# Optimization experiments

Measured on AMD Instinct MI355X. Metric: run time of the kernel, lower is better.

Reference implementation:

```python
import jax, jax.numpy as jnp
import numpy as np

EPS = 1e-6
ROPE_BASE = 10000.0


def rms_norm(x, gamma):
    # normalize over last dim (head_dim)
    var = jnp.mean(x * x, axis=-1, keepdims=True)
    return x * jax.lax.rsqrt(var + EPS) * gamma


def apply_rope(x):
    # x: [B, L, nH, hd]; rotate-half RoPE over flattened sequence positions
    L, hd = x.shape[1], x.shape[-1]
    half = hd // 2
    inv_freq = 1.0 / (ROPE_BASE ** (jnp.arange(half, dtype=jnp.float32) / half))
    ang = jnp.arange(L, dtype=jnp.float32)[:, None] * inv_freq[None, :]  # [L, half]
    cos = jnp.cos(ang)[None, :, None, :]
    sin = jnp.sin(ang)[None, :, None, :]
    x1, x2 = x[..., :half], x[..., half:]
    return jnp.concatenate([x1 * cos - x2 * sin, x1 * sin + x2 * cos], axis=-1)


def setup_inputs() -> dict:
    key = jax.random.key(0)
    k1, k2, k3 = jax.random.split(key, 3)
    B, H, W, C = 8, 32, 32, 768
    x = jax.random.normal(k1, (B, H, W, C), dtype=jnp.float32)
    w_qkv = jax.random.normal(k2, (3 * C, C), dtype=jnp.float32) * (1.0 / np.sqrt(C))
    w_out = jax.random.normal(k3, (C, C), dtype=jnp.float32) * (1.0 / np.sqrt(C))
    q_gamma = jnp.ones((64,), dtype=jnp.float32)
    k_gamma = jnp.ones((64,), dtype=jnp.float32)
    return {"x": x, "w_qkv": w_qkv, "q_gamma": q_gamma, "k_gamma": k_gamma, "w_out": w_out}


def reference(x, w_qkv, q_gamma, k_gamma, w_out):
    B, H, W, C = x.shape
    nH = 12
    hd = C // nH
    L = H * W
    x_flat = x.reshape(B, L, C)
    qkv = jnp.einsum('blc,dc->bld', x_flat, w_qkv).reshape(B, L, 3, nH, hd)
    q, k, v = qkv[:, :, 0], qkv[:, :, 1], qkv[:, :, 2]  # [B, L, nH, hd]
    q = apply_rope(rms_norm(q, q_gamma))
    k = apply_rope(rms_norm(k, k_gamma))
    scale = 1.0 / np.sqrt(hd)
    scores = jnp.einsum('bqhd,bkhd->bhqk', q, k) * scale
    attn = jax.nn.softmax(scores, axis=-1)
    out = jnp.einsum('bhqk,bkhd->bqhd', attn, v).reshape(B, H, W, C)
    return jnp.einsum('bhwc,dc->bhwd', out, w_out)
```

## Files before the change

kernel.cpp:

```cpp
#include <hip/hip_runtime.h>
#include <math.h>

#define NB 8
#define SL 1024
#define CD 768
#define NHH 12
#define HD 64
#define QKVD 2304

typedef __attribute__((ext_vector_type(8))) __bf16 bf16x8;
typedef __attribute__((ext_vector_type(8))) unsigned short u16x8;
typedef __attribute__((ext_vector_type(4))) float f32x4;
typedef __attribute__((ext_vector_type(16))) float f32x16;
typedef __attribute__((ext_vector_type(4))) unsigned int u32x4;
#define MFMA16(a, b, c) __builtin_amdgcn_mfma_f32_16x16x32_bf16(a, b, c, 0, 0, 0)
#define MFMA32(a, b, c) __builtin_amdgcn_mfma_f32_32x32x16_bf16(a, b, c, 0, 0, 0)

__host__ __device__ __forceinline__ float bf2f(unsigned short u) {
  union { unsigned int i; float f; } v; v.i = ((unsigned int)u) << 16; return v.f;
}
__host__ __device__ __forceinline__ unsigned short f2bf(float f) {
  union { float ff; unsigned int i; } v; v.ff = f;
  unsigned int x = v.i;
  x += 0x7FFFu + ((x >> 16) & 1u);
  return (unsigned short)(x >> 16);
}
__device__ __forceinline__ unsigned int pkbf(float a, float b) {
  unsigned short ua = __builtin_bit_cast(unsigned short, (__bf16)a);
  unsigned short ub = __builtin_bit_cast(unsigned short, (__bf16)b);
  return ((unsigned int)ub << 16) | ua;
}

__device__ __forceinline__ void gload_lds16(const void* g, void* l) {
  __builtin_amdgcn_global_load_lds(
      (const __attribute__((address_space(1))) unsigned int*)g,
      (__attribute__((address_space(3))) unsigned int*)l, 16, 0, 0);
}

__global__ __launch_bounds__(256) void conv_kernel(
    const float4* __restrict__ in, ushort4* __restrict__ out, int n4)
{
  int i = blockIdx.x * 256 + threadIdx.x;
  if (i < n4) {
    float4 v = in[i];
    ushort4 o;
    o.x = f2bf(v.x); o.y = f2bf(v.y); o.z = f2bf(v.z); o.w = f2bf(v.w);
    out[i] = o;
  }
}

template <int CF32>
__global__ __launch_bounds__(256) void gemm_mfma(
    const unsigned short* __restrict__ A, const unsigned short* __restrict__ B,
    void* __restrict__ Cv, int M, int N, int K)
{
  __shared__ alignas(16) unsigned short AsL[128 * 32];
  __shared__ alignas(16) unsigned short BsL[128 * 32];
  const int m0 = blockIdx.y * 128, n0 = blockIdx.x * 128;
  const int t = threadIdx.x;
  const int wave = t >> 6, lane = t & 63;
  const int wm = (wave >> 1) * 64, wn = (wave & 1) * 64;
  const int lm = lane & 15, quad = lane >> 4;
  f32x4 acc[4][4];
#pragma unroll
  for (int i = 0; i < 4; ++i)
#pragma unroll
    for (int j = 0; j < 4; ++j)
#pragma unroll
      for (int r = 0; r < 4; ++r) acc[i][j][r] = 0.f;

  const int sr = t >> 2, sc = (t & 3) * 8;
  const unsigned short* ag = A + (size_t)(m0 + sr) * K + sc;
  const unsigned short* bg = B + (size_t)(n0 + sr) * K + sc;
  for (int k0 = 0; k0 < K; k0 += 32) {
    gload_lds16(ag + k0, &AsL[t * 8]);
    gload_lds16(ag + (size_t)64 * K + k0, &AsL[2048 + t * 8]);
    gload_lds16(bg + k0, &BsL[t * 8]);
    gload_lds16(bg + (size_t)64 * K + k0, &BsL[2048 + t * 8]);
    __syncthreads();
    bf16x8 af[4], bfr[4];
#pragma unroll
    for (int i = 0; i < 4; ++i)
      af[i] = *(const bf16x8*)&AsL[(wm + i * 16 + lm) * 32 + quad * 8];
#pragma unroll
    for (int j = 0; j < 4; ++j)
      bfr[j] = *(const bf16x8*)&BsL[(wn + j * 16 + lm) * 32 + quad * 8];
#pragma unroll
    for (int i = 0; i < 4; ++i)
#pragma unroll
      for (int j = 0; j < 4; ++j)
        acc[i][j] = MFMA16(af[i], bfr[j], acc[i][j]);
    __syncthreads();
  }
#pragma unroll
  for (int i = 0; i < 4; ++i) {
    const int row = m0 + wm + i * 16 + quad * 4;
#pragma unroll
    for (int r = 0; r < 4; ++r) {
      const size_t base = (size_t)(row + r) * N + n0 + wn + lm;
#pragma unroll
      for (int j = 0; j < 4; ++j) {
        if (CF32) ((float*)Cv)[base + j * 16] = acc[i][j][r];
        else ((unsigned short*)Cv)[base + j * 16] = f2bf(acc[i][j][r]);
      }
    }
  }
}

__global__ __launch_bounds__(256) void rmsrope_kernel(
    unsigned short* __restrict__ qkv,
    const float* __restrict__ qg, const float* __restrict__ kg)
{
  const int wid  = (int)((blockIdx.x * blockDim.x + threadIdx.x) >> 6);
  const int lane = threadIdx.x & 63;
  const int h = wid % NHH;
  const int s = (wid / NHH) & 1;
  const int l = (wid / (2 * NHH)) % SL;
  const int b = wid / (2 * NHH * SL);
  unsigned short* p = qkv + (((size_t)(b * SL + l) * 3 + s) * NHH + h) * HD + lane;
  float v = bf2f(*p);
  float ss = v * v;
#pragma unroll
  for (int off = 32; off; off >>= 1) ss += __shfl_xor(ss, off);
  float g = s ? kg[lane] : qg[lane];
  v = v * rsqrtf(ss * (1.0f / 64.0f) + 1e-6f) * g;
  float partner = __shfl_xor(v, 32);
  const int j = lane & 31;
  float ang = (float)l * exp2f((float)j * (-13.287712379549449f / 32.0f));
  float sn, cs;
  sincosf(ang, &sn, &cs);
  *p = f2bf((lane < 32) ? (v * cs - partner * sn) : (partner * sn + v * cs));
}

__global__ __launch_bounds__(256) void attn_mfma(
    const unsigned short* __restrict__ qkv, unsigned short* __restrict__ ctx)
{
  __shared__ alignas(16) unsigned short KsL[2][64 * 64];
  __shared__ alignas(16) unsigned short Vt[2][64][76];
  const int bid = (int)(blockIdx.x + 8 * (blockIdx.y + 12 * blockIdx.z));
  const int nb = (bid & 7) * 96 + (bid >> 3);
  const int qt = nb & 7;
  const int h = (nb >> 3) % 12;
  const int b = nb / 96;
  const int t = threadIdx.x, wave = t >> 6, lane = t & 63;
  const int q_l = lane & 31, hi = lane >> 5;
  const int wq = wave * 32;
  const int vkey = t & 63, vds = (t >> 6) * 16;
  const int kr = t >> 3, kc = t & 7;
  const float SCALE = 0.125f * 1.44269504088896340736f;

  const unsigned short* base_k = qkv + (size_t)b * SL * QKVD + (NHH * HD) + h * HD;
  const unsigned short* base_v = qkv + (size_t)b * SL * QKVD + 2 * (NHH * HD) + h * HD;

  bf16x8 qf[4];
  {
    const unsigned short* qp =
        qkv + (((size_t)(b * SL + qt * 128 + wq + q_l) * 3 + 0) * NHH + h) * HD + hi * 8;
#pragma unroll
    for (int ds = 0; ds < 4; ++ds) qf[ds] = *(const bf16x8*)(qp + ds * 16);
  }
  f32x16 o0, o1;
#pragma unroll
  for (int r = 0; r < 16; ++r) { o0[r] = 0.f; o1[r] = 0.f; }
  float m_i = -INFINITY, l_i = 0.f;

  const int ksw = (kc ^ (kr & 7)) * 8;
#define STAGE_K(KT, BUF)                                                      \
  {                                                                           \
    const unsigned short* k0p = base_k + (size_t)((KT)*64 + kr) * QKVD + ksw; \
    gload_lds16(k0p, &KsL[BUF][t * 8]);                                       \
    const unsigned short* k1p =                                               \
        base_k + (size_t)((KT)*64 + 32 + kr) * QKVD + ksw;                    \
    gload_lds16(k1p, &KsL[BUF][2048 + t * 8]);                                \
  }

  STAGE_K(0, 0);
  {
    const unsigned short* vp = base_v + (size_t)vkey * QKVD + vds;
    u16x8 v0 = *(const u16x8*)(vp);
    u16x8 v1 = *(const u16x8*)(vp + 8);
#pragma unroll
    for (int e = 0; e < 8; ++e) {
      Vt[0][vds + e][vkey] = v0[e];
      Vt[0][vds + 8 + e][vkey] = v1[e];
    }
  }
  __syncthreads();

  for (int kt = 0; kt < 16; ++kt) {
    const int cur = kt & 1, nxt = cur ^ 1;
    const int ktn = (kt + 1) & 15;
    STAGE_K(ktn, nxt);
    const unsigned short* vp = base_v + (size_t)(ktn * 64 + vkey) * QKVD + vds;
    u16x8 v0n = *(const u16x8*)(vp);
    u16x8 v1n = *(const u16x8*)(vp + 8);
    const unsigned short* Kb = KsL[cur];
    f32x16 st0, st1;
#pragma unroll
    for (int r = 0; r < 16; ++r) { st0[r] = 0.f; st1[r] = 0.f; }
#pragma unroll
    for (int ds = 0; ds < 4; ++ds) {
      const int c = 2 * ds + hi;
      bf16x8 k0 = *(const bf16x8*)&Kb[q_l * 64 + ((c ^ (q_l & 7)) * 8)];
      bf16x8 k1 = *(const bf16x8*)&Kb[(32 + q_l) * 64 + ((c ^ (q_l & 7)) * 8)];
      st0 = MFMA32(k0, qf[ds], st0);
      st1 = MFMA32(k1, qf[ds], st1);
    }
    float tm = -INFINITY;
#pragma unroll
    for (int r = 0; r < 16; ++r) {
      st0[r] *= SCALE; st1[r] *= SCALE;
      tm = fmaxf(tm, fmaxf(st0[r], st1[r]));
    }
    tm = fmaxf(tm, __shfl_xor(tm, 32));
    const float mn = fmaxf(m_i, tm);
    const float al = __builtin_amdgcn_exp2f(m_i - mn);
    m_i = mn;
    float rs = 0.f;
#pragma unroll
    for (int r = 0; r < 16; ++r) {
      st0[r] = __builtin_amdgcn_exp2f(st0[r] - mn);
      st1[r] = __builtin_amdgcn_exp2f(st1[r] - mn);
      rs += st0[r] + st1[r];
    }
    rs += __shfl_xor(rs, 32);
    l_i = l_i * al + rs;
#pragma unroll
    for (int r = 0; r < 16; ++r) { o0[r] *= al; o1[r] *= al; }
#define PV_KS(KS, PVEC, RL)                                              \
    {                                                                    \
      unsigned int a0 = pkbf(PVEC[RL + 0], PVEC[RL + 1]);                \
      unsigned int a1 = pkbf(PVEC[RL + 2], PVEC[RL + 3]);                \
      unsigned int b0 = pkbf(PVEC[RL + 4], PVEC[RL + 5]);                \
      unsigned int b1 = pkbf(PVEC[RL + 6], PVEC[RL + 7]);                \
      unsigned int s0 = hi ? a0 : b0, s1 = hi ? a1 : b1;                 \
      unsigned int r0 = __shfl_xor(s0, 32), r1 = __shfl_xor(s1, 32);     \
      u32x4 pw;                                                          \
      pw[0] = hi ? r0 : a0; pw[1] = hi ? r1 : a1;                        \
      pw[2] = hi ? b0 : r0; pw[3] = hi ? b1 : r1;                        \
      bf16x8 paf = __builtin_bit_cast(bf16x8, pw);                       \
      bf16x8 v0f = *(const bf16x8*)&Vt[cur][q_l][(KS)*16 + hi * 8];      \
      bf16x8 v1f = *(const bf16x8*)&Vt[cur][32 + q_l][(KS)*16 + hi * 8]; \
      o0 = MFMA32(v0f, paf, o0);                                         \
      o1 = MFMA32(v1f, paf, o1);                                         \
    }
    PV_KS(0, st0, 0)
    PV_KS(1, st0, 8)
    PV_KS(2, st1, 0)
    PV_KS(3, st1, 8)
#undef PV_KS
#pragma unroll
    for (int e = 0; e < 8; ++e) {
      Vt[nxt][vds + e][vkey] = v0n[e];
      Vt[nxt][vds + 8 + e][vkey] = v1n[e];
    }
    __syncthreads();
  }
  const float inv = 1.f / l_i;
  const size_t row = (size_t)(b * SL + qt * 128 + wq + q_l) * CD + h * HD;
#pragma unroll
  for (int g = 0; g < 4; ++g) {
    uint2 w0, w1;
    w0.x = pkbf(o0[4 * g + 0] * inv, o0[4 * g + 1] * inv);
    w0.y = pkbf(o0[4 * g + 2] * inv, o0[4 * g + 3] * inv);
    *(uint2*)&ctx[row + 8 * g + 4 * hi] = w0;
    w1.x = pkbf(o1[4 * g + 0] * inv, o1[4 * g + 1] * inv);
    w1.y = pkbf(o1[4 * g + 2] * inv, o1[4 * g + 3] * inv);
    *(uint2*)&ctx[row + 32 + 8 * g + 4 * hi] = w1;
  }
#undef STAGE_K
}

extern "C" void kernel_launch(void* const* d_in, const int* in_sizes, int n_in,
                              void* d_out, int out_size, void* d_ws, size_t ws_size,
                              hipStream_t stream) {
  const float* x     = (const float*)d_in[0];
  const float* w_qkv = (const float*)d_in[1];
  const float* qg    = (const float*)d_in[2];
  const float* kg    = (const float*)d_in[3];
  const float* w_out = (const float*)d_in[4];

  unsigned short* xb  = (unsigned short*)d_ws;
  unsigned short* wqb = xb + (size_t)NB * SL * CD;
  unsigned short* wob = wqb + (size_t)QKVD * CD;
  unsigned short* qkv = wob + (size_t)CD * CD;
  unsigned short* ctx = qkv + (size_t)NB * SL * QKVD;

  const int M = NB * SL;
  dim3 blk(256);
  conv_kernel<<<dim3(M * CD / 4 / 256), blk, 0, stream>>>(
      (const float4*)x, (ushort4*)xb, M * CD / 4);
  conv_kernel<<<dim3(QKVD * CD / 4 / 256), blk, 0, stream>>>(
      (const float4*)w_qkv, (ushort4*)wqb, QKVD * CD / 4);
  conv_kernel<<<dim3(CD * CD / 4 / 256), blk, 0, stream>>>(
      (const float4*)w_out, (ushort4*)wob, CD * CD / 4);
  gemm_mfma<0><<<dim3(QKVD / 128, M / 128), blk, 0, stream>>>(
      xb, wqb, qkv, M, QKVD, CD);
  rmsrope_kernel<<<dim3(NB * SL * 2 * NHH / 4), blk, 0, stream>>>(qkv, qg, kg);
  attn_mfma<<<dim3(SL / 128, NHH, NB), blk, 0, stream>>>(qkv, ctx);
  gemm_mfma<1><<<dim3(CD / 128, M / 128), blk, 0, stream>>>(
      ctx, wob, d_out, M, CD, CD);
}
```

Measured before the change: 245.7 us.

## Fuse RMSNorm+RoPE into QKV GEMM epilogue and add lazy softmax rescale

The QKV GEMM now applies RMSNorm and RoPE in its epilogue for the q and k column ranges, using 16-lane shuffle reductions over each 64-wide head tile. This removes the separate rmsrope kernel and its extra read and write of q/k. The attention kernel also skips the running-max rescale of o and l unless the new max exceeds the old one by more than 8 (log2 units), folds the scale into an fma before exp2, and raises wave priority around the MFMA sections. The deferred rescale lets exponentials grow by up to 2^8 before renormalisation, and the fused epilogue adds sincos work and register pressure to the GEMM.

```diff
diff --git a/kernel.cpp b/kernel.cpp
--- a/kernel.cpp
+++ b/kernel.cpp
@@ -49,10 +49,11 @@
   }
 }
 
-template <int CF32>
+template <int MODE>
 __global__ __launch_bounds__(256) void gemm_mfma(
     const unsigned short* __restrict__ A, const unsigned short* __restrict__ B,
-    void* __restrict__ Cv, int M, int N, int K)
+    void* __restrict__ Cv, int M, int N, int K,
+    const float* __restrict__ qg, const float* __restrict__ kg)
 {
   __shared__ alignas(16) unsigned short AsL[128 * 32];
   __shared__ alignas(16) unsigned short BsL[128 * 32];
@@ -92,6 +93,43 @@
         acc[i][j] = MFMA16(af[i], bfr[j], acc[i][j]);
     __syncthreads();
   }
+
+  if (MODE == 2 && (n0 + wn) < 2 * CD) {
+    const float* gam = ((n0 + wn) >= CD) ? kg : qg;
+    float g4[4];
+#pragma unroll
+    for (int j = 0; j < 4; ++j) g4[j] = gam[j * 16 + lm];
+    const float C1 = -13.287712379549449f / 32.0f;
+    const float if0 = exp2f((float)lm * C1);
+    const float if1 = exp2f((float)(16 + lm) * C1);
+    unsigned short* Cs = (unsigned short*)Cv;
+#pragma unroll
+    for (int i = 0; i < 4; ++i) {
+      const int row = m0 + wm + i * 16 + quad * 4;
+#pragma unroll
+      for (int r = 0; r < 4; ++r) {
+        float v0 = acc[i][0][r], v1 = acc[i][1][r];
+        float v2 = acc[i][2][r], v3 = acc[i][3][r];
+        float ssq = v0 * v0 + v1 * v1 + v2 * v2 + v3 * v3;
+#pragma unroll
+        for (int off = 8; off; off >>= 1) ssq += __shfl_xor(ssq, off);
+        const float sc2 = rsqrtf(ssq * (1.0f / 64.0f) + 1e-6f);
+        v0 *= sc2 * g4[0]; v1 *= sc2 * g4[1];
+        v2 *= sc2 * g4[2]; v3 *= sc2 * g4[3];
+        const int l = (row + r) & (SL - 1);
+        float sn0, cs0, sn1, cs1;
+        sincosf((float)l * if0, &sn0, &cs0);
+        sincosf((float)l * if1, &sn1, &cs1);
+        const size_t base = (size_t)(row + r) * N + n0 + wn + lm;
+        Cs[base +  0] = f2bf(v0 * cs0 - v2 * sn0);
+        Cs[base + 16] = f2bf(v1 * cs1 - v3 * sn1);
+        Cs[base + 32] = f2bf(v0 * sn0 + v2 * cs0);
+        Cs[base + 48] = f2bf(v1 * sn1 + v3 * cs1);
+      }
+    }
+    return;
+  }
+
 #pragma unroll
   for (int i = 0; i < 4; ++i) {
     const int row = m0 + wm + i * 16 + quad * 4;
@@ -100,36 +138,11 @@
       const size_t base = (size_t)(row + r) * N + n0 + wn + lm;
 #pragma unroll
       for (int j = 0; j < 4; ++j) {
-        if (CF32) ((float*)Cv)[base + j * 16] = acc[i][j][r];
+        if (MODE == 1) ((float*)Cv)[base + j * 16] = acc[i][j][r];
         else ((unsigned short*)Cv)[base + j * 16] = f2bf(acc[i][j][r]);
       }
     }
   }
-}
-
-__global__ __launch_bounds__(256) void rmsrope_kernel(
-    unsigned short* __restrict__ qkv,
-    const float* __restrict__ qg, const float* __restrict__ kg)
-{
-  const int wid  = (int)((blockIdx.x * blockDim.x + threadIdx.x) >> 6);
-  const int lane = threadIdx.x & 63;
-  const int h = wid % NHH;
-  const int s = (wid / NHH) & 1;
-  const int l = (wid / (2 * NHH)) % SL;
-  const int b = wid / (2 * NHH * SL);
-  unsigned short* p = qkv + (((size_t)(b * SL + l) * 3 + s) * NHH + h) * HD + lane;
-  float v = bf2f(*p);
-  float ss = v * v;
-#pragma unroll
-  for (int off = 32; off; off >>= 1) ss += __shfl_xor(ss, off);
-  float g = s ? kg[lane] : qg[lane];
-  v = v * rsqrtf(ss * (1.0f / 64.0f) + 1e-6f) * g;
-  float partner = __shfl_xor(v, 32);
-  const int j = lane & 31;
-  float ang = (float)l * exp2f((float)j * (-13.287712379549449f / 32.0f));
-  float sn, cs;
-  sincosf(ang, &sn, &cs);
-  *p = f2bf((lane < 32) ? (v * cs - partner * sn) : (partner * sn + v * cs));
 }
 
 __global__ __launch_bounds__(256) void attn_mfma(
@@ -198,6 +211,7 @@
     f32x16 st0, st1;
 #pragma unroll
     for (int r = 0; r < 16; ++r) { st0[r] = 0.f; st1[r] = 0.f; }
+    __builtin_amdgcn_s_setprio(1);
 #pragma unroll
     for (int ds = 0; ds < 4; ++ds) {
       const int c = 2 * ds + hi;
@@ -206,27 +220,35 @@
       st0 = MFMA32(k0, qf[ds], st0);
       st1 = MFMA32(k1, qf[ds], st1);
     }
-    float tm = -INFINITY;
+    __builtin_amdgcn_s_setprio(0);
+    float t0 = fmaxf(st0[0], st1[0]), t1 = fmaxf(st0[1], st1[1]);
+    float t2 = fmaxf(st0[2], st1[2]), t3 = fmaxf(st0[3], st1[3]);
+#pragma unroll
+    for (int r = 4; r < 16; r += 4) {
+      t0 = fmaxf(t0, fmaxf(st0[r + 0], st1[r + 0]));
+      t1 = fmaxf(t1, fmaxf(st0[r + 1], st1[r + 1]));
+      t2 = fmaxf(t2, fmaxf(st0[r + 2], st1[r + 2]));
+      t3 = fmaxf(t3, fmaxf(st0[r + 3], st1[r + 3]));
+    }
+    float tm = fmaxf(fmaxf(t0, t1), fmaxf(t2, t3)) * SCALE;
+    tm = fmaxf(tm, __shfl_xor(tm, 32));
+    if (!__all(tm - m_i <= 8.0f)) {
+      const float mn = fmaxf(m_i, tm);
+      const float al = __builtin_amdgcn_exp2f(m_i - mn);
+      m_i = mn;
+      l_i *= al;
+#pragma unroll
+      for (int r = 0; r < 16; ++r) { o0[r] *= al; o1[r] *= al; }
+    }
+    float rs = 0.f;
 #pragma unroll
     for (int r = 0; r < 16; ++r) {
-      st0[r] *= SCALE; st1[r] *= SCALE;
-      tm = fmaxf(tm, fmaxf(st0[r], st1[r]));
-    }
-    tm = fmaxf(tm, __shfl_xor(tm, 32));
-    const float mn = fmaxf(m_i, tm);
-    const float al = __builtin_amdgcn_exp2f(m_i - mn);
-    m_i = mn;
-    float rs = 0.f;
-#pragma unroll
-    for (int r = 0; r < 16; ++r) {
-      st0[r] = __builtin_amdgcn_exp2f(st0[r] - mn);
-      st1[r] = __builtin_amdgcn_exp2f(st1[r] - mn);
+      st0[r] = __builtin_amdgcn_exp2f(fmaf(st0[r], SCALE, -m_i));
+      st1[r] = __builtin_amdgcn_exp2f(fmaf(st1[r], SCALE, -m_i));
       rs += st0[r] + st1[r];
     }
     rs += __shfl_xor(rs, 32);
-    l_i = l_i * al + rs;
-#pragma unroll
-    for (int r = 0; r < 16; ++r) { o0[r] *= al; o1[r] *= al; }
+    l_i += rs;
 #define PV_KS(KS, PVEC, RL)                                              \
     {                                                                    \
       unsigned int a0 = pkbf(PVEC[RL + 0], PVEC[RL + 1]);                \
@@ -241,8 +263,10 @@
       bf16x8 paf = __builtin_bit_cast(bf16x8, pw);                       \
       bf16x8 v0f = *(const bf16x8*)&Vt[cur][q_l][(KS)*16 + hi * 8];      \
       bf16x8 v1f = *(const bf16x8*)&Vt[cur][32 + q_l][(KS)*16 + hi * 8]; \
+      __builtin_amdgcn_s_setprio(1);                                     \
       o0 = MFMA32(v0f, paf, o0);                                         \
       o1 = MFMA32(v1f, paf, o1);                                         \
+      __builtin_amdgcn_s_setprio(0);                                     \
     }
     PV_KS(0, st0, 0)
     PV_KS(1, st0, 8)
@@ -294,10 +318,9 @@
       (const float4*)w_qkv, (ushort4*)wqb, QKVD * CD / 4);
   conv_kernel<<<dim3(CD * CD / 4 / 256), blk, 0, stream>>>(
       (const float4*)w_out, (ushort4*)wob, CD * CD / 4);
-  gemm_mfma<0><<<dim3(QKVD / 128, M / 128), blk, 0, stream>>>(
-      xb, wqb, qkv, M, QKVD, CD);
-  rmsrope_kernel<<<dim3(NB * SL * 2 * NHH / 4), blk, 0, stream>>>(qkv, qg, kg);
+  gemm_mfma<2><<<dim3(QKVD / 128, M / 128), blk, 0, stream>>>(
+      xb, wqb, qkv, M, QKVD, CD, qg, kg);
   attn_mfma<<<dim3(SL / 128, NHH, NB), blk, 0, stream>>>(qkv, ctx);
   gemm_mfma<1><<<dim3(CD / 128, M / 128), blk, 0, stream>>>(
-      ctx, wob, d_out, M, CD, CD);
-}
+      ctx, wob, d_out, M, CD, CD, nullptr, nullptr);
+}
```

Measured after the change: 244.8 us. About the same (-0.4%).
